# Performance work log

Hardware: AMD Instinct MI355X
Metric: run time of the kernel (lower is better)

Reference implementation:

```python
import jax, jax.numpy as jnp
import numpy as np

UPS_MEL = 100   # mel frame -> samples
UPS_LOW = 10    # lowres -> samples
H = 512         # GRU hidden
MEL = 80
LC = 20         # lowres conv channels
PRE = 256
SS = 30         # MOL sample_size (10 mixtures x 3)


def setup_inputs() -> dict:
    key = jax.random.key(0)
    ks = jax.random.split(key, 16)
    B, TM, TL = 8, 80, 800
    T = TM * UPS_MEL  # 8000
    rn = lambda k, s, sc=1.0: jax.random.normal(k, s, dtype=jnp.float32) * sc
    z = lambda n: jnp.zeros((n,), dtype=jnp.float32)
    return {
        "mel": rn(ks[0], (B, TM, MEL)),
        "x_low": rn(ks[1], (B, TL), 0.5),
        "gs_x": rn(ks[2], (B, T), 0.5),
        "conv_w0": rn(ks[3], (LC, 1, 7), 0.3),
        "conv_b0": z(LC),
        "conv_w1": rn(ks[4], (LC, LC, 7), 0.1),
        "conv_b1": z(LC),
        "conv_w2": rn(ks[5], (LC, LC, 7), 0.1),
        "conv_b2": z(LC),
        "gru_wih0": rn(ks[6], (3 * H, 102), 0.05),
        "gru_whh0": rn(ks[7], (3 * H, H), 0.05),
        "gru_bih0": z(3 * H),
        "gru_bhh0": z(3 * H),
        "gru_wih1": rn(ks[8], (3 * H, H), 0.05),
        "gru_whh1": rn(ks[9], (3 * H, H), 0.05),
        "gru_bih1": z(3 * H),
        "gru_bhh1": z(3 * H),
        "pre_w": rn(ks[10], (PRE, H), 0.05),
        "pre_b": z(PRE),
        "out_w": rn(ks[11], (SS, PRE), 0.05),
        "out_b": z(SS),
    }


def _lin_interp(x, out_len):
    # torch F.interpolate(mode='linear', align_corners=False) on [B, L] -> [B, out_len]
    L = x.shape[1]
    src = (jnp.arange(out_len, dtype=jnp.float32) + 0.5) * (L / out_len) - 0.5
    src = jnp.clip(src, 0.0, L - 1)
    i0 = jnp.floor(src).astype(jnp.int32)
    i1 = jnp.minimum(i0 + 1, L - 1)
    w = src - i0.astype(jnp.float32)
    return x[:, i0] * (1.0 - w) + x[:, i1] * w


def _conv1d(x, w, b):
    # x: [B, C, L], w: [O, I, K], 'same' padding (K=7 -> pad 3)
    k = w.shape[-1]
    p = (k - 1) // 2
    y = jax.lax.conv_general_dilated(x, w, (1,), [(p, p)],
                                     dimension_numbers=("NCH", "OIH", "NCH"))
    return y + b[None, :, None]


def _gru(x, wih, whh, bih, bhh):
    # x: [B, T, I] -> [B, T, H]; PyTorch GRU gate math, h0 = 0
    B = x.shape[0]
    xg = jnp.einsum("bti,gi->btg", x, wih) + bih  # [B, T, 3H]
    h0 = jnp.zeros((B, H), dtype=x.dtype)

    def step(h, xg_t):
        hg = h @ whh.T + bhh
        xr, xz, xn = jnp.split(xg_t, 3, axis=-1)
        hr, hz, hn = jnp.split(hg, 3, axis=-1)
        r = jax.nn.sigmoid(xr + hr)
        z = jax.nn.sigmoid(xz + hz)
        n = jnp.tanh(xn + r * hn)
        h_new = (1.0 - z) * n + z * h
        return h_new, h_new

    _, hs = jax.lax.scan(step, h0, jnp.swapaxes(xg, 0, 1))
    return jnp.swapaxes(hs, 0, 1)


def reference(mel, x_low, gs_x,
              conv_w0, conv_b0, conv_w1, conv_b1, conv_w2, conv_b2,
              gru_wih0, gru_whh0, gru_bih0, gru_bhh0,
              gru_wih1, gru_whh1, gru_bih1, gru_bhh1,
              pre_w, pre_b, out_w, out_b):
    # UpsampleNetR on mel: repeat each frame UPS_MEL times -> [B, T, 80]
    up_mel = jnp.repeat(mel, UPS_MEL, axis=1)
    # UpsampleNetI on x_low: linear interp x UPS_LOW -> [B, TL*10]
    interp_x = _lin_interp(x_low, x_low.shape[1] * UPS_LOW)
    # lowres conv stack with tanh: [B, 1, TL] -> [B, 20, TL]
    h = x_low[:, None, :]
    for w, b in ((conv_w0, conv_b0), (conv_w1, conv_b1), (conv_w2, conv_b2)):
        h = jnp.tanh(_conv1d(h, w, b))
    # UpsampleNetR on conv features: [B, TL, 20] repeated x10 -> [B, TL*10, 20]
    up_x = jnp.repeat(jnp.swapaxes(h, 1, 2), UPS_LOW, axis=1)

    msize = min(up_mel.shape[1], gs_x.shape[1], up_x.shape[1], interp_x.shape[1])
    hidden = jnp.concatenate([up_mel[:, :msize, :], up_x[:, :msize, :],
                              interp_x[:, :msize, None], gs_x[:, :msize, None]],
                             axis=-1)  # [B, T, 102]

    hidden = _gru(hidden, gru_wih0, gru_whh0, gru_bih0, gru_bhh0)
    hidden = _gru(hidden, gru_wih1, gru_whh1, gru_bih1, gru_bhh1)

    pre = jnp.tanh(hidden @ pre_w.T + pre_b)   # [B, T, 256]
    return pre @ out_w.T + out_b               # [B, T, 30]
```

## Files before the change

### kernel.cpp

```cpp
#include <hip/hip_runtime.h>
#include <hip/hip_fp16.h>
#include <stdint.h>

#define TT     8000
#define TLOW   800
#define TMEL   80
#define NMEL   80
#define NB     8
#define HD     512
#define LC     20
#define NPRE   256
#define NSS    30

#define HB_SLOTS (TT + 1)
#define HB_U64   ((size_t)HB_SLOTS * 8 * 128)
#define HB_BYTES (HB_U64 * 8)
#define CONV_BYTES   ((size_t)NB * TLOW * LC * 4)
#define INTERP_BYTES ((size_t)NB * TT * 4)
#define PREW16_BYTES ((size_t)NPRE * HD * 2)
#define OUTW16_BYTES ((size_t)NSS * NPRE * 2)

typedef __attribute__((ext_vector_type(8))) _Float16 half8;
typedef __attribute__((ext_vector_type(4))) float f32x4;

static __device__ __forceinline__ unsigned short f2h_bits(float f) {
    union { _Float16 h; unsigned short u; } c; c.h = (_Float16)f; return c.u;
}
static __device__ __forceinline__ float sigf(float x) {
    x = fminf(30.f, fmaxf(-30.f, x));
    return 1.f / (1.f + __expf(-x));
}
static __device__ __forceinline__ float tanhf_(float x) {
    x = fminf(15.f, fmaxf(-15.f, x));
    float e = __expf(2.f * x);
    return (e - 1.f) / (e + 1.f);
}
static __device__ __forceinline__ half8 mkfrag(unsigned long long a, unsigned long long b) {
    union { unsigned long long q[2]; half8 v; } u; u.q[0] = a; u.q[1] = b; return u.v;
}
static __device__ __forceinline__ f32x4 mfma(half8 a, half8 b, f32x4 c) {
    return __builtin_amdgcn_mfma_f32_16x16x32_f16(a, b, c, 0, 0, 0);
}

static __device__ __forceinline__ void issue16(const unsigned long long* __restrict__ p,
                                               int lane, unsigned long long* __restrict__ q)
{
    #pragma unroll
    for (int k = 0; k < 16; k++)
        q[k] = __hip_atomic_load(p + lane + 64 * k, __ATOMIC_RELAXED, __HIP_MEMORY_SCOPE_AGENT);
}
static __device__ __forceinline__ bool good16(const unsigned long long* __restrict__ q)
{
    bool bad = false;
    #pragma unroll
    for (int k = 0; k < 16; k++) {
        unsigned int lo = (unsigned int)q[k], hi = (unsigned int)(q[k] >> 32);
        bad |= (lo == 0xFFFFFFFFu) | (hi == 0xFFFFFFFFu);
    }
    return !__any(bad);
}
static __device__ __forceinline__ void stage16(unsigned long long* __restrict__ st,
                                               int lane, const unsigned long long* __restrict__ q)
{
    #pragma unroll
    for (int k = 0; k < 16; k++) { int i = lane + 64 * k; st[(i >> 7) * 129 + (i & 127)] = q[k]; }
}
static __device__ void poll_hot(const unsigned long long* __restrict__ slot,
                                int lane, unsigned long long* __restrict__ st)
{
    unsigned long long a[16], b[16];
    issue16(slot, lane, a);
    issue16(slot, lane, b);
    for (;;) {
        if (good16(a)) { stage16(st, lane, a); return; }
        issue16(slot, lane, a);
        if (good16(b)) { stage16(st, lane, b); return; }
        issue16(slot, lane, b);
    }
}
static __device__ void poll_sleep(const unsigned long long* __restrict__ slot,
                                  int lane, unsigned long long* __restrict__ st)
{
    unsigned long long a[16];
    for (;;) {
        issue16(slot, lane, a);
        if (good16(a)) break;
        __builtin_amdgcn_s_sleep(1);
    }
    stage16(st, lane, a);
}
static __device__ __forceinline__ half8 ldsfrag(const unsigned long long* __restrict__ st,
                                                int lane, int kt)
{
    int base = (lane & 7) * 129 + ((lane >> 4) << 1) + kt * 8;
    return mkfrag(st[base], st[base + 1]);
}

__global__ __launch_bounds__(256) void k_prep(
    const float* __restrict__ pre_w, const float* __restrict__ out_w,
    unsigned short* __restrict__ prew16, unsigned short* __restrict__ outw16)
{
    int i = blockIdx.x * 256 + threadIdx.x;
    if (i < NPRE * HD) prew16[i] = f2h_bits(pre_w[i]);
    if (i < NSS * NPRE) outw16[i] = f2h_bits(out_w[i]);
}

#define CHW 218
__global__ __launch_bounds__(256) void k_conv(
    const float* __restrict__ xlow,
    const float* __restrict__ w0, const float* __restrict__ cb0,
    const float* __restrict__ w1, const float* __restrict__ cb1,
    const float* __restrict__ w2, const float* __restrict__ cb2,
    float* __restrict__ convout, float* __restrict__ interp)
{
    int blk = blockIdx.x; int b = blk >> 2; int ch = blk & 3; int cb = ch * 200;
    int tid = threadIdx.x;
    __shared__ float xr[224];
    __shared__ float w0l[LC * 7], w1l[LC * LC * 7], w2l[LC * LC * 7];
    __shared__ float b0l[LC], b1l[LC], b2l[LC];
    __shared__ float h0[LC][CHW], h1[LC][CHW];

    for (int i = tid; i < LC * 7; i += 256) w0l[i] = w0[i];
    for (int i = tid; i < LC * LC * 7; i += 256) { w1l[i] = w1[i]; w2l[i] = w2[i]; }
    for (int i = tid; i < LC; i += 256) { b0l[i] = cb0[i]; b1l[i] = cb1[i]; b2l[i] = cb2[i]; }
    for (int i = tid; i < 224; i += 256) {
        int g = cb - 12 + i;
        xr[i] = (g >= 0 && g < TLOW) ? xlow[b * TLOW + g] : 0.f;
    }
    __syncthreads();
    for (int i = tid; i < LC * CHW; i += 256) {
        int c = i / CHW, s = i - c * CHW;
        int tg = cb - 9 + s;
        float a = b0l[c];
        #pragma unroll
        for (int j = 0; j < 7; j++) a += w0l[c * 7 + j] * xr[s + j];
        h0[c][s] = (tg >= 0 && tg < TLOW) ? tanhf_(a) : 0.f;
    }
    __syncthreads();
    for (int i = tid; i < LC * CHW; i += 256) {
        int c = i / CHW, s = i - c * CHW;
        int tg = cb - 9 + s;
        float a = b1l[c];
        for (int ci = 0; ci < LC; ci++) {
            #pragma unroll
            for (int j = 0; j < 7; j++) {
                int ss = s + j - 3;
                float hv = (ss >= 0 && ss < CHW) ? h0[ci][ss] : 0.f;
                a += w1l[(c * LC + ci) * 7 + j] * hv;
            }
        }
        h1[c][s] = (tg >= 0 && tg < TLOW) ? tanhf_(a) : 0.f;
    }
    __syncthreads();
    for (int i = tid; i < LC * 200; i += 256) {
        int c = i / 200, t0 = i - c * 200; int s = t0 + 9;
        float a = b2l[c];
        for (int ci = 0; ci < LC; ci++) {
            #pragma unroll
            for (int j = 0; j < 7; j++) a += w2l[(c * LC + ci) * 7 + j] * h1[ci][s + j - 3];
        }
        convout[((size_t)b * TLOW + cb + t0) * LC + c] = tanhf_(a);
    }
    for (int i = tid; i < 2000; i += 256) {
        int t = cb * 10 + i;
        float src = ((float)t + 0.5f) * 0.1f - 0.5f;
        src = fminf(fmaxf(src, 0.f), (float)(TLOW - 1));
        int i0 = (int)floorf(src); int i1 = (i0 + 1 < TLOW) ? i0 + 1 : TLOW - 1;
        float w = src - (float)i0;
        interp[(size_t)b * TT + t] = xlow[b * TLOW + i0] * (1.f - w) + xlow[b * TLOW + i1] * w;
    }
}

__global__ __launch_bounds__(384, 1) void k_rnn(
    const float* __restrict__ mel, const float* __restrict__ gsx,
    const float* __restrict__ convout, const float* __restrict__ interp,
    const float* __restrict__ wih0, const float* __restrict__ whh0,
    const float* __restrict__ bih0, const float* __restrict__ bhh0,
    const float* __restrict__ wih1, const float* __restrict__ whh1,
    const float* __restrict__ bih1, const float* __restrict__ bhh1,
    unsigned long long* __restrict__ h0buf, unsigned long long* __restrict__ h1buf)
{
    const int tid = threadIdx.x;
    const int wv = tid >> 6;
    const int lane = tid & 63;
    const int lm = lane & 15, lk = lane >> 4;
    const int g = wv >> 1;
    const int isH = wv & 1;
    const bool isL0 = (blockIdx.x < 32);
    const int cbid = isL0 ? blockIdx.x : (blockIdx.x - 32);
    const int cb = cbid * 16;
    const int row = g * 512 + cb + lm;

    __shared__ float exch[3][2][16][9];
    __shared__ __align__(16) unsigned short xv[2][16][136];
    __shared__ unsigned long long stX[8 * 129];
    __shared__ unsigned long long stH[8 * 129];

    const int cbb = lane >> 3;
    const int ci0 = (lane & 7) * 2, ci1 = ci0 + 1;
    float hr0 = 0.f, hr1 = 0.f;
    float bi0[3], bi1[3], bh0[3], bh1[3];
    if (wv == 0) {
        const float* bi = isL0 ? bih0 : bih1;
        const float* bh = isL0 ? bhh0 : bhh1;
        #pragma unroll
        for (int gg = 0; gg < 3; gg++) {
            bi0[gg] = bi[gg * 512 + cb + ci0]; bi1[gg] = bi[gg * 512 + cb + ci1];
            bh0[gg] = bh[gg * 512 + cb + ci0]; bh1[gg] = bh[gg * 512 + cb + ci1];
        }
    }
    for (int i = tid; i < 2 * 16 * 136; i += 384) (&xv[0][0][0])[i] = 0;

    if (wv == 0) {
        unsigned long long* buf = isL0 ? h0buf : h1buf;
        unsigned int* o32 = (unsigned int*)buf + (size_t)cbb * 256 + (cb >> 1) + (lane & 7);
        __hip_atomic_store(o32, 0u, __ATOMIC_RELAXED, __HIP_MEMORY_SCOPE_AGENT);
    }

    half8 wf[16];
    if (isL0) {
        if (!isH) {
            #pragma unroll
            for (int kt = 0; kt < 4; kt++)
                #pragma unroll
                for (int j = 0; j < 8; j++) {
                    int k = kt * 32 + lk * 8 + j;
                    wf[kt][j] = (k < 102) ? (_Float16)wih0[(size_t)row * 102 + k] : (_Float16)0.f;
                }
        } else {
            #pragma unroll
            for (int kt = 0; kt < 16; kt++)
                #pragma unroll
                for (int j = 0; j < 8; j++)
                    wf[kt][j] = (_Float16)whh0[(size_t)row * 512 + kt * 32 + lk * 8 + j];
        }
    } else {
        const float* wsrc = isH ? whh1 : wih1;
        #pragma unroll
        for (int kt = 0; kt < 16; kt++)
            #pragma unroll
            for (int j = 0; j < 8; j++)
                wf[kt][j] = (_Float16)wsrc[(size_t)row * 512 + kt * 32 + lk * 8 + j];
    }

    if (isL0) {
        {
            float pf[3];
            #pragma unroll
            for (int u = 0; u < 3; u++) {
                int e = tid + 384 * u; float v = 0.f;
                if (e < 816) {
                    int bb = e / 102, k = e - 102 * bb;
                    if (k < 80)       v = mel[((size_t)bb * TMEL + 0) * NMEL + k];
                    else if (k < 100) v = convout[((size_t)bb * TLOW + 0) * LC + (k - 80)];
                    else if (k == 100) v = interp[(size_t)bb * TT + 0];
                    else               v = gsx[(size_t)bb * TT + 0];
                }
                pf[u] = v;
            }
            #pragma unroll
            for (int u = 0; u < 3; u++) {
                int e = tid + 384 * u;
                if (e < 816) { int bb = e / 102, k = e - 102 * bb; xv[0][bb][k] = f2h_bits(pf[u]); }
            }
        }
        __syncthreads();

        for (int t = 0; t < TT; t++) {
            int tn = (t + 1 < TT) ? (t + 1) : (TT - 1);
            int tmi = tn / 100, tli = tn / 10;
            float pf[3];
            #pragma unroll
            for (int u = 0; u < 3; u++) {
                int e = tid + 384 * u; float v = 0.f;
                if (e < 816) {
                    int bb = e / 102, k = e - 102 * bb;
                    if (k < 80)       v = mel[((size_t)bb * TMEL + tmi) * NMEL + k];
                    else if (k < 100) v = convout[((size_t)bb * TLOW + tli) * LC + (k - 80)];
                    else if (k == 100) v = interp[(size_t)bb * TT + tn];
                    else               v = gsx[(size_t)bb * TT + tn];
                }
                pf[u] = v;
            }

            if (wv == 1) poll_hot(h0buf + (size_t)t * 1024, lane, stH);
            __syncthreads();

            if (!isH) {
                f32x4 acc = {0.f, 0.f, 0.f, 0.f};
                #pragma unroll
                for (int kt = 0; kt < 4; kt++) {
                    half8 xf = *(const half8*)&xv[t & 1][lm][kt * 32 + lk * 8];
                    acc = mfma(wf[kt], xf, acc);
                }
                if (lm < 8) {
                    #pragma unroll
                    for (int r2 = 0; r2 < 4; r2++) exch[g][0][lk * 4 + r2][lm] = acc[r2];
                }
            } else {
                f32x4 a0 = {0.f, 0.f, 0.f, 0.f}, a1 = {0.f, 0.f, 0.f, 0.f};
                #pragma unroll
                for (int i = 0; i < 8; i++) a0 = mfma(wf[i], ldsfrag(stH, lane, i), a0);
                #pragma unroll
                for (int i = 0; i < 8; i++) a1 = mfma(wf[8 + i], ldsfrag(stH, lane, 8 + i), a1);
                f32x4 acc = a0 + a1;
                if (lm < 8) {
                    #pragma unroll
                    for (int r2 = 0; r2 < 4; r2++) exch[g][1][lk * 4 + r2][lm] = acc[r2];
                }
            }
            #pragma unroll
            for (int u = 0; u < 3; u++) {
                int e = tid + 384 * u;
                if (e < 816) { int bb = e / 102, k = e - 102 * bb; xv[(t + 1) & 1][bb][k] = f2h_bits(pf[u]); }
            }
            __syncthreads();
            if (wv == 0) {
                float r0 = sigf(exch[0][0][ci0][cbb] + exch[0][1][ci0][cbb] + bi0[0] + bh0[0]);
                float z0 = sigf(exch[1][0][ci0][cbb] + exch[1][1][ci0][cbb] + bi0[1] + bh0[1]);
                float n0 = tanhf_(exch[2][0][ci0][cbb] + bi0[2] + r0 * (exch[2][1][ci0][cbb] + bh0[2]));
                hr0 = (1.f - z0) * n0 + z0 * hr0;
                float r1 = sigf(exch[0][0][ci1][cbb] + exch[0][1][ci1][cbb] + bi1[0] + bh1[0]);
                float z1 = sigf(exch[1][0][ci1][cbb] + exch[1][1][ci1][cbb] + bi1[1] + bh1[1]);
                float n1 = tanhf_(exch[2][0][ci1][cbb] + bi1[2] + r1 * (exch[2][1][ci1][cbb] + bh1[2]));
                hr1 = (1.f - z1) * n1 + z1 * hr1;
                unsigned int pk = (unsigned int)f2h_bits(hr0) | ((unsigned int)f2h_bits(hr1) << 16);
                unsigned int* o32 = (unsigned int*)(h0buf + (size_t)(t + 1) * 1024)
                                  + (size_t)cbb * 256 + (cb >> 1) + (lane & 7);
                __hip_atomic_store(o32, pk, __ATOMIC_RELAXED, __HIP_MEMORY_SCOPE_AGENT);
            }
        }
    } else {
        __syncthreads();
        for (int t = 0; t < TT; t++) {
            if (wv == 0)      poll_sleep(h0buf + (size_t)(t + 1) * 1024, lane, stX);
            else if (wv == 1) poll_hot(h1buf + (size_t)t * 1024, lane, stH);
            __syncthreads();

            const unsigned long long* src = isH ? stH : stX;
            f32x4 a0 = {0.f, 0.f, 0.f, 0.f}, a1 = {0.f, 0.f, 0.f, 0.f};
            #pragma unroll
            for (int i = 0; i < 8; i++) a0 = mfma(wf[i], ldsfrag(src, lane, i), a0);
            #pragma unroll
            for (int i = 0; i < 8; i++) a1 = mfma(wf[8 + i], ldsfrag(src, lane, 8 + i), a1);
            f32x4 acc = a0 + a1;
            if (lm < 8) {
                #pragma unroll
                for (int r2 = 0; r2 < 4; r2++) exch[g][isH][lk * 4 + r2][lm] = acc[r2];
            }
            __syncthreads();
            if (wv == 0) {
                float r0 = sigf(exch[0][0][ci0][cbb] + exch[0][1][ci0][cbb] + bi0[0] + bh0[0]);
                float z0 = sigf(exch[1][0][ci0][cbb] + exch[1][1][ci0][cbb] + bi0[1] + bh0[1]);
                float n0 = tanhf_(exch[2][0][ci0][cbb] + bi0[2] + r0 * (exch[2][1][ci0][cbb] + bh0[2]));
                hr0 = (1.f - z0) * n0 + z0 * hr0;
                float r1 = sigf(exch[0][0][ci1][cbb] + exch[0][1][ci1][cbb] + bi1[0] + bh1[0]);
                float z1 = sigf(exch[1][0][ci1][cbb] + exch[1][1][ci1][cbb] + bi1[1] + bh1[1]);
                float n1 = tanhf_(exch[2][0][ci1][cbb] + bi1[2] + r1 * (exch[2][1][ci1][cbb] + bh1[2]));
                hr1 = (1.f - z1) * n1 + z1 * hr1;
                unsigned int pk = (unsigned int)f2h_bits(hr0) | ((unsigned int)f2h_bits(hr1) << 16);
                unsigned int* o32 = (unsigned int*)(h1buf + (size_t)(t + 1) * 1024)
                                  + (size_t)cbb * 256 + (cb >> 1) + (lane & 7);
                __hip_atomic_store(o32, pk, __ATOMIC_RELAXED, __HIP_MEMORY_SCOPE_AGENT);
            }
        }
    }
}

__global__ __launch_bounds__(256) void k_final(
    const unsigned long long* __restrict__ h1buf,
    const unsigned short* __restrict__ prew16, const float* __restrict__ pre_b,
    const unsigned short* __restrict__ outw16, const float* __restrict__ out_b,
    float* __restrict__ out)
{
    int blk = blockIdx.x; int b = blk / 125; int tb = (blk - b * 125) * 64;
    int tid = threadIdx.x; int wv = tid >> 6; int l = tid & 63;
    int lm = l & 15, lk = l >> 4;

    half8 af[16];
    int trow = tb + wv * 16 + lm;
    const unsigned long long* abase = h1buf + ((size_t)(trow + 1) * 8 + b) * 128;
    #pragma unroll
    for (int kt = 0; kt < 16; kt++)
        af[kt] = mkfrag(abase[kt * 8 + lk * 2], abase[kt * 8 + lk * 2 + 1]);

    f32x4 acc[16];
    #pragma unroll
    for (int nt = 0; nt < 16; nt++) {
        f32x4 z = {0.f, 0.f, 0.f, 0.f}; acc[nt] = z;
        #pragma unroll
        for (int kt = 0; kt < 16; kt++) {
            int n = nt * 16 + lm; int k = kt * 32 + lk * 8;
            half8 bw = *(const half8*)&prew16[(size_t)n * HD + k];
            acc[nt] = mfma(af[kt], bw, acc[nt]);
        }
    }
    __shared__ __align__(16) unsigned short pt[64][264];
    #pragma unroll
    for (int nt = 0; nt < 16; nt++) {
        float pb = pre_b[nt * 16 + lm];
        #pragma unroll
        for (int r2 = 0; r2 < 4; r2++)
            pt[wv * 16 + lk * 4 + r2][nt * 16 + lm] = f2h_bits(tanhf_(acc[nt][r2] + pb));
    }
    __syncthreads();
    f32x4 a2[2];
    { f32x4 z = {0.f, 0.f, 0.f, 0.f}; a2[0] = z; a2[1] = z; }
    #pragma unroll
    for (int kt = 0; kt < 8; kt++) {
        half8 pa = *(const half8*)&pt[wv * 16 + lm][kt * 32 + lk * 8];
        #pragma unroll
        for (int nt = 0; nt < 2; nt++) {
            int n = nt * 16 + lm;
            half8 bw = (n < NSS) ? *(const half8*)&outw16[(size_t)n * NPRE + kt * 32 + lk * 8]
                                 : mkfrag(0ull, 0ull);
            a2[nt] = mfma(pa, bw, a2[nt]);
        }
    }
    #pragma unroll
    for (int nt = 0; nt < 2; nt++) {
        int n = nt * 16 + lm;
        if (n < NSS) {
            float ob = out_b[n];
            #pragma unroll
            for (int r2 = 0; r2 < 4; r2++) {
                int t = tb + wv * 16 + lk * 4 + r2;
                out[((size_t)b * TT + t) * NSS + n] = a2[nt][r2] + ob;
            }
        }
    }
}

extern "C" void kernel_launch(void* const* d_in, const int* in_sizes, int n_in,
                              void* d_out, int out_size, void* d_ws, size_t ws_size,
                              hipStream_t stream) {
    const float* mel  = (const float*)d_in[0];
    const float* xlow = (const float*)d_in[1];
    const float* gsx  = (const float*)d_in[2];
    const float* cw0  = (const float*)d_in[3];
    const float* cb0  = (const float*)d_in[4];
    const float* cw1  = (const float*)d_in[5];
    const float* cb1  = (const float*)d_in[6];
    const float* cw2  = (const float*)d_in[7];
    const float* cb2  = (const float*)d_in[8];
    const float* wih0 = (const float*)d_in[9];
    const float* whh0 = (const float*)d_in[10];
    const float* bih0 = (const float*)d_in[11];
    const float* bhh0 = (const float*)d_in[12];
    const float* wih1 = (const float*)d_in[13];
    const float* whh1 = (const float*)d_in[14];
    const float* bih1 = (const float*)d_in[15];
    const float* bhh1 = (const float*)d_in[16];
    const float* prew = (const float*)d_in[17];
    const float* preb = (const float*)d_in[18];
    const float* outw = (const float*)d_in[19];
    const float* outb = (const float*)d_in[20];

    size_t needed = 2 * HB_BYTES + CONV_BYTES + INTERP_BYTES + PREW16_BYTES + OUTW16_BYTES;
    if (ws_size < needed) return;

    char* ws = (char*)d_ws;
    unsigned long long* h0buf = (unsigned long long*)ws;
    unsigned long long* h1buf = (unsigned long long*)(ws + HB_BYTES);
    float* convout = (float*)(ws + 2 * HB_BYTES);
    float* interp  = (float*)(ws + 2 * HB_BYTES + CONV_BYTES);
    unsigned short* prew16 = (unsigned short*)(ws + 2 * HB_BYTES + CONV_BYTES + INTERP_BYTES);
    unsigned short* outw16 = (unsigned short*)(ws + 2 * HB_BYTES + CONV_BYTES + INTERP_BYTES + PREW16_BYTES);

    hipMemsetAsync(ws, 0xFF, 2 * HB_BYTES, stream);

    k_prep<<<(NPRE * HD + 255) / 256, 256, 0, stream>>>(prew, outw, prew16, outw16);
    k_conv<<<32, 256, 0, stream>>>(xlow, cw0, cb0, cw1, cb1, cw2, cb2, convout, interp);
    k_rnn<<<64, 384, 0, stream>>>(mel, gsx, convout, interp,
                                  wih0, whh0, bih0, bhh0,
                                  wih1, whh1, bih1, bhh1,
                                  h0buf, h1buf);
    k_final<<<1000, 256, 0, stream>>>(h1buf, prew16, preb, outw16, outb, (float*)d_out);
}
```

Before: 21.18 ms.

## Halve RNN block count with 32-column blocks and rebalanced MFMA work split

The persistent GRU kernel moves from 64 blocks of 384 threads, each owning 16 hidden columns, to 32 blocks of 768 threads, each owning 32 columns. In layer 0 the input projection and the recurrent K dimension are split more evenly across waves, with a third partial-sum slot in the exchange buffer. The hot double-buffered poller is replaced by a single sleeping poller. Fewer blocks means fewer producers and consumers on the cross-block handshake each step, but per-block barriers now cover more waves and the sleep-based polling may add latency.

```diff
diff --git a/kernel.cpp b/kernel.cpp
--- a/kernel.cpp
+++ b/kernel.cpp
@@ -59,35 +59,17 @@
     }
     return !__any(bad);
 }
-static __device__ __forceinline__ void stage16(unsigned long long* __restrict__ st,
-                                               int lane, const unsigned long long* __restrict__ q)
-{
+static __device__ void poll_stage(const unsigned long long* __restrict__ slot,
+                                  int lane, unsigned long long* __restrict__ st)
+{
+    unsigned long long q[16];
+    for (;;) {
+        issue16(slot, lane, q);
+        if (good16(q)) break;
+        __builtin_amdgcn_s_sleep(1);
+    }
     #pragma unroll
     for (int k = 0; k < 16; k++) { int i = lane + 64 * k; st[(i >> 7) * 129 + (i & 127)] = q[k]; }
-}
-static __device__ void poll_hot(const unsigned long long* __restrict__ slot,
-                                int lane, unsigned long long* __restrict__ st)
-{
-    unsigned long long a[16], b[16];
-    issue16(slot, lane, a);
-    issue16(slot, lane, b);
-    for (;;) {
-        if (good16(a)) { stage16(st, lane, a); return; }
-        issue16(slot, lane, a);
-        if (good16(b)) { stage16(st, lane, b); return; }
-        issue16(slot, lane, b);
-    }
-}
-static __device__ void poll_sleep(const unsigned long long* __restrict__ slot,
-                                  int lane, unsigned long long* __restrict__ st)
-{
-    unsigned long long a[16];
-    for (;;) {
-        issue16(slot, lane, a);
-        if (good16(a)) break;
-        __builtin_amdgcn_s_sleep(1);
-    }
-    stage16(st, lane, a);
 }
 static __device__ __forceinline__ half8 ldsfrag(const unsigned long long* __restrict__ st,
                                                 int lane, int kt)
@@ -171,7 +153,7 @@
     }
 }
 
-__global__ __launch_bounds__(384, 1) void k_rnn(
+__global__ __launch_bounds__(768, 1) void k_rnn(
     const float* __restrict__ mel, const float* __restrict__ gsx,
     const float* __restrict__ convout, const float* __restrict__ interp,
     const float* __restrict__ wih0, const float* __restrict__ whh0,
@@ -184,71 +166,59 @@
     const int wv = tid >> 6;
     const int lane = tid & 63;
     const int lm = lane & 15, lk = lane >> 4;
-    const int g = wv >> 1;
-    const int isH = wv & 1;
-    const bool isL0 = (blockIdx.x < 32);
-    const int cbid = isL0 ? blockIdx.x : (blockIdx.x - 32);
-    const int cb = cbid * 16;
-    const int row = g * 512 + cb + lm;
-
-    __shared__ float exch[3][2][16][9];
+    const int g = wv >> 2;
+    const int sub = wv & 3;
+    const bool isL0 = (blockIdx.x < 16);
+    const int cbid = isL0 ? blockIdx.x : (blockIdx.x - 16);
+    const int cb = cbid * 32;
+
+    __shared__ float exch[3][3][32][9];
     __shared__ __align__(16) unsigned short xv[2][16][136];
     __shared__ unsigned long long stX[8 * 129];
     __shared__ unsigned long long stH[8 * 129];
 
     const int cbb = lane >> 3;
-    const int ci0 = (lane & 7) * 2, ci1 = ci0 + 1;
+    const int ci0 = wv * 16 + (lane & 7) * 2;
     float hr0 = 0.f, hr1 = 0.f;
     float bi0[3], bi1[3], bh0[3], bh1[3];
-    if (wv == 0) {
+    if (wv < 2) {
         const float* bi = isL0 ? bih0 : bih1;
         const float* bh = isL0 ? bhh0 : bhh1;
         #pragma unroll
         for (int gg = 0; gg < 3; gg++) {
-            bi0[gg] = bi[gg * 512 + cb + ci0]; bi1[gg] = bi[gg * 512 + cb + ci1];
-            bh0[gg] = bh[gg * 512 + cb + ci0]; bh1[gg] = bh[gg * 512 + cb + ci1];
-        }
-    }
-    for (int i = tid; i < 2 * 16 * 136; i += 384) (&xv[0][0][0])[i] = 0;
-
-    if (wv == 0) {
+            bi0[gg] = bi[gg * 512 + cb + ci0];     bi1[gg] = bi[gg * 512 + cb + ci0 + 1];
+            bh0[gg] = bh[gg * 512 + cb + ci0];     bh1[gg] = bh[gg * 512 + cb + ci0 + 1];
+        }
+    }
+    for (int i = tid; i < 2 * 16 * 136; i += 768) (&xv[0][0][0])[i] = 0;
+
+    if (wv < 2) {
         unsigned long long* buf = isL0 ? h0buf : h1buf;
-        unsigned int* o32 = (unsigned int*)buf + (size_t)cbb * 256 + (cb >> 1) + (lane & 7);
+        unsigned int* o32 = (unsigned int*)buf + (size_t)cbb * 256 + cbid * 16 + wv * 8 + (lane & 7);
         __hip_atomic_store(o32, 0u, __ATOMIC_RELAXED, __HIP_MEMORY_SCOPE_AGENT);
     }
 
-    half8 wf[16];
     if (isL0) {
-        if (!isH) {
-            #pragma unroll
-            for (int kt = 0; kt < 4; kt++)
-                #pragma unroll
-                for (int j = 0; j < 8; j++) {
-                    int k = kt * 32 + lk * 8 + j;
-                    wf[kt][j] = (k < 102) ? (_Float16)wih0[(size_t)row * 102 + k] : (_Float16)0.f;
-                }
-        } else {
-            #pragma unroll
-            for (int kt = 0; kt < 16; kt++)
-                #pragma unroll
-                for (int j = 0; j < 8; j++)
-                    wf[kt][j] = (_Float16)whh0[(size_t)row * 512 + kt * 32 + lk * 8 + j];
-        }
-    } else {
-        const float* wsrc = isH ? whh1 : wih1;
-        #pragma unroll
-        for (int kt = 0; kt < 16; kt++)
-            #pragma unroll
-            for (int j = 0; j < 8; j++)
-                wf[kt][j] = (_Float16)wsrc[(size_t)row * 512 + kt * 32 + lk * 8 + j];
-    }
-
-    if (isL0) {
+        const int mt = sub >> 1, kh = sub & 1;
+        const int row = g * 512 + cb + mt * 16 + lm;
+        half8 wf[10];
+        #pragma unroll
+        for (int q = 0; q < 10; q++) {
+            #pragma unroll
+            for (int j = 0; j < 8; j++) {
+                float v;
+                if (kh == 0) {
+                    if (q < 4) { int k = q * 32 + lk * 8 + j; v = (k < 102) ? wih0[(size_t)row * 102 + k] : 0.f; }
+                    else       { int k = (q - 4) * 32 + lk * 8 + j; v = whh0[(size_t)row * 512 + k]; }
+                } else       { int k = (q + 6) * 32 + lk * 8 + j; v = whh0[(size_t)row * 512 + k]; }
+                wf[q][j] = (_Float16)v;
+            }
+        }
         {
-            float pf[3];
-            #pragma unroll
-            for (int u = 0; u < 3; u++) {
-                int e = tid + 384 * u; float v = 0.f;
+            float pf[2];
+            #pragma unroll
+            for (int u = 0; u < 2; u++) {
+                int e = tid + 768 * u; float v = 0.f;
                 if (e < 816) {
                     int bb = e / 102, k = e - 102 * bb;
                     if (k < 80)       v = mel[((size_t)bb * TMEL + 0) * NMEL + k];
@@ -259,8 +229,8 @@
                 pf[u] = v;
             }
             #pragma unroll
-            for (int u = 0; u < 3; u++) {
-                int e = tid + 384 * u;
+            for (int u = 0; u < 2; u++) {
+                int e = tid + 768 * u;
                 if (e < 816) { int bb = e / 102, k = e - 102 * bb; xv[0][bb][k] = f2h_bits(pf[u]); }
             }
         }
@@ -269,10 +239,10 @@
         for (int t = 0; t < TT; t++) {
             int tn = (t + 1 < TT) ? (t + 1) : (TT - 1);
             int tmi = tn / 100, tli = tn / 10;
-            float pf[3];
-            #pragma unroll
-            for (int u = 0; u < 3; u++) {
-                int e = tid + 384 * u; float v = 0.f;
+            float pf[2];
+            #pragma unroll
+            for (int u = 0; u < 2; u++) {
+                int e = tid + 768 * u; float v = 0.f;
                 if (e < 816) {
                     int bb = e / 102, k = e - 102 * bb;
                     if (k < 80)       v = mel[((size_t)bb * TMEL + tmi) * NMEL + k];
@@ -283,84 +253,103 @@
                 pf[u] = v;
             }
 
-            if (wv == 1) poll_hot(h0buf + (size_t)t * 1024, lane, stH);
+            if (wv == 3) poll_stage(h0buf + (size_t)t * 1024, lane, stH);
             __syncthreads();
 
-            if (!isH) {
-                f32x4 acc = {0.f, 0.f, 0.f, 0.f};
+            if (kh == 0) {
+                f32x4 aX = {0.f, 0.f, 0.f, 0.f}, aH = {0.f, 0.f, 0.f, 0.f};
                 #pragma unroll
-                for (int kt = 0; kt < 4; kt++) {
-                    half8 xf = *(const half8*)&xv[t & 1][lm][kt * 32 + lk * 8];
-                    acc = mfma(wf[kt], xf, acc);
+                for (int q = 0; q < 4; q++) {
+                    half8 xf = *(const half8*)&xv[t & 1][lm][q * 32 + lk * 8];
+                    aX = mfma(wf[q], xf, aX);
                 }
+                #pragma unroll
+                for (int q = 0; q < 6; q++) aH = mfma(wf[4 + q], ldsfrag(stH, lane, q), aH);
                 if (lm < 8) {
                     #pragma unroll
-                    for (int r2 = 0; r2 < 4; r2++) exch[g][0][lk * 4 + r2][lm] = acc[r2];
+                    for (int r2 = 0; r2 < 4; r2++) {
+                        exch[g][0][mt * 16 + lk * 4 + r2][lm] = aX[r2];
+                        exch[g][1][mt * 16 + lk * 4 + r2][lm] = aH[r2];
+                    }
                 }
             } else {
-                f32x4 a0 = {0.f, 0.f, 0.f, 0.f}, a1 = {0.f, 0.f, 0.f, 0.f};
+                f32x4 aH = {0.f, 0.f, 0.f, 0.f}, aH2 = {0.f, 0.f, 0.f, 0.f};
                 #pragma unroll
-                for (int i = 0; i < 8; i++) a0 = mfma(wf[i], ldsfrag(stH, lane, i), a0);
+                for (int q = 0; q < 5; q++) aH = mfma(wf[q], ldsfrag(stH, lane, 6 + q), aH);
                 #pragma unroll
-                for (int i = 0; i < 8; i++) a1 = mfma(wf[8 + i], ldsfrag(stH, lane, 8 + i), a1);
-                f32x4 acc = a0 + a1;
+                for (int q = 5; q < 10; q++) aH2 = mfma(wf[q], ldsfrag(stH, lane, 6 + q), aH2);
+                aH = aH + aH2;
                 if (lm < 8) {
                     #pragma unroll
-                    for (int r2 = 0; r2 < 4; r2++) exch[g][1][lk * 4 + r2][lm] = acc[r2];
+                    for (int r2 = 0; r2 < 4; r2++) exch[g][2][mt * 16 + lk * 4 + r2][lm] = aH[r2];
                 }
             }
             #pragma unroll
-            for (int u = 0; u < 3; u++) {
-                int e = tid + 384 * u;
+            for (int u = 0; u < 2; u++) {
+                int e = tid + 768 * u;
                 if (e < 816) { int bb = e / 102, k = e - 102 * bb; xv[(t + 1) & 1][bb][k] = f2h_bits(pf[u]); }
             }
             __syncthreads();
-            if (wv == 0) {
+            if (wv < 2) {
+                float r0 = sigf(exch[0][0][ci0][cbb] + exch[0][1][ci0][cbb] + exch[0][2][ci0][cbb] + bi0[0] + bh0[0]);
+                float z0 = sigf(exch[1][0][ci0][cbb] + exch[1][1][ci0][cbb] + exch[1][2][ci0][cbb] + bi0[1] + bh0[1]);
+                float n0 = tanhf_(exch[2][0][ci0][cbb] + bi0[2]
+                                  + r0 * (exch[2][1][ci0][cbb] + exch[2][2][ci0][cbb] + bh0[2]));
+                hr0 = (1.f - z0) * n0 + z0 * hr0;
+                int i1 = ci0 + 1;
+                float r1 = sigf(exch[0][0][i1][cbb] + exch[0][1][i1][cbb] + exch[0][2][i1][cbb] + bi1[0] + bh1[0]);
+                float z1 = sigf(exch[1][0][i1][cbb] + exch[1][1][i1][cbb] + exch[1][2][i1][cbb] + bi1[1] + bh1[1]);
+                float n1 = tanhf_(exch[2][0][i1][cbb] + bi1[2]
+                                  + r1 * (exch[2][1][i1][cbb] + exch[2][2][i1][cbb] + bh1[2]));
+                hr1 = (1.f - z1) * n1 + z1 * hr1;
+                unsigned int pk = (unsigned int)f2h_bits(hr0) | ((unsigned int)f2h_bits(hr1) << 16);
+                unsigned int* o32 = (unsigned int*)(h0buf + (size_t)(t + 1) * 1024)
+                                  + (size_t)cbb * 256 + cbid * 16 + wv * 8 + (lane & 7);
+                __hip_atomic_store(o32, pk, __ATOMIC_RELAXED, __HIP_MEMORY_SCOPE_AGENT);
+            }
+        }
+    } else {
+        const int isH = sub >> 1, mt = sub & 1;
+        const int row = g * 512 + cb + mt * 16 + lm;
+        const float* wsrc = isH ? whh1 : wih1;
+        half8 wf[16];
+        #pragma unroll
+        for (int q = 0; q < 16; q++)
+            #pragma unroll
+            for (int j = 0; j < 8; j++)
+                wf[q][j] = (_Float16)wsrc[(size_t)row * 512 + q * 32 + lk * 8 + j];
+        __syncthreads();
+
+        for (int t = 0; t < TT; t++) {
+            if (wv == 2)      poll_stage(h0buf + (size_t)(t + 1) * 1024, lane, stX);
+            else if (wv == 3) poll_stage(h1buf + (size_t)t * 1024,       lane, stH);
+            __syncthreads();
+
+            const unsigned long long* src = isH ? stH : stX;
+            f32x4 a0 = {0.f, 0.f, 0.f, 0.f}, a1 = {0.f, 0.f, 0.f, 0.f};
+            #pragma unroll
+            for (int q = 0; q < 8; q++) a0 = mfma(wf[q], ldsfrag(src, lane, q), a0);
+            #pragma unroll
+            for (int q = 8; q < 16; q++) a1 = mfma(wf[q], ldsfrag(src, lane, q), a1);
+            f32x4 acc = a0 + a1;
+            if (lm < 8) {
+                #pragma unroll
+                for (int r2 = 0; r2 < 4; r2++) exch[g][isH][mt * 16 + lk * 4 + r2][lm] = acc[r2];
+            }
+            __syncthreads();
+            if (wv < 2) {
                 float r0 = sigf(exch[0][0][ci0][cbb] + exch[0][1][ci0][cbb] + bi0[0] + bh0[0]);
                 float z0 = sigf(exch[1][0][ci0][cbb] + exch[1][1][ci0][cbb] + bi0[1] + bh0[1]);
                 float n0 = tanhf_(exch[2][0][ci0][cbb] + bi0[2] + r0 * (exch[2][1][ci0][cbb] + bh0[2]));
                 hr0 = (1.f - z0) * n0 + z0 * hr0;
-                float r1 = sigf(exch[0][0][ci1][cbb] + exch[0][1][ci1][cbb] + bi1[0] + bh1[0]);
-                float z1 = sigf(exch[1][0][ci1][cbb] + exch[1][1][ci1][cbb] + bi1[1] + bh1[1]);
-                float n1 = tanhf_(exch[2][0][ci1][cbb] + bi1[2] + r1 * (exch[2][1][ci1][cbb] + bh1[2]));
-                hr1 = (1.f - z1) * n1 + z1 * hr1;
-                unsigned int pk = (unsigned int)f2h_bits(hr0) | ((unsigned int)f2h_bits(hr1) << 16);
-                unsigned int* o32 = (unsigned int*)(h0buf + (size_t)(t + 1) * 1024)
-                                  + (size_t)cbb * 256 + (cb >> 1) + (lane & 7);
-                __hip_atomic_store(o32, pk, __ATOMIC_RELAXED, __HIP_MEMORY_SCOPE_AGENT);
-            }
-        }
-    } else {
-        __syncthreads();
-        for (int t = 0; t < TT; t++) {
-            if (wv == 0)      poll_sleep(h0buf + (size_t)(t + 1) * 1024, lane, stX);
-            else if (wv == 1) poll_hot(h1buf + (size_t)t * 1024, lane, stH);
-            __syncthreads();
-
-            const unsigned long long* src = isH ? stH : stX;
-            f32x4 a0 = {0.f, 0.f, 0.f, 0.f}, a1 = {0.f, 0.f, 0.f, 0.f};
-            #pragma unroll
-            for (int i = 0; i < 8; i++) a0 = mfma(wf[i], ldsfrag(src, lane, i), a0);
-            #pragma unroll
-            for (int i = 0; i < 8; i++) a1 = mfma(wf[8 + i], ldsfrag(src, lane, 8 + i), a1);
-            f32x4 acc = a0 + a1;
-            if (lm < 8) {
-                #pragma unroll
-                for (int r2 = 0; r2 < 4; r2++) exch[g][isH][lk * 4 + r2][lm] = acc[r2];
-            }
-            __syncthreads();
-            if (wv == 0) {
-                float r0 = sigf(exch[0][0][ci0][cbb] + exch[0][1][ci0][cbb] + bi0[0] + bh0[0]);
-                float z0 = sigf(exch[1][0][ci0][cbb] + exch[1][1][ci0][cbb] + bi0[1] + bh0[1]);
-                float n0 = tanhf_(exch[2][0][ci0][cbb] + bi0[2] + r0 * (exch[2][1][ci0][cbb] + bh0[2]));
-                hr0 = (1.f - z0) * n0 + z0 * hr0;
-                float r1 = sigf(exch[0][0][ci1][cbb] + exch[0][1][ci1][cbb] + bi1[0] + bh1[0]);
-                float z1 = sigf(exch[1][0][ci1][cbb] + exch[1][1][ci1][cbb] + bi1[1] + bh1[1]);
-                float n1 = tanhf_(exch[2][0][ci1][cbb] + bi1[2] + r1 * (exch[2][1][ci1][cbb] + bh1[2]));
+                int i1 = ci0 + 1;
+                float r1 = sigf(exch[0][0][i1][cbb] + exch[0][1][i1][cbb] + bi1[0] + bh1[0]);
+                float z1 = sigf(exch[1][0][i1][cbb] + exch[1][1][i1][cbb] + bi1[1] + bh1[1]);
+                float n1 = tanhf_(exch[2][0][i1][cbb] + bi1[2] + r1 * (exch[2][1][i1][cbb] + bh1[2]));
                 hr1 = (1.f - z1) * n1 + z1 * hr1;
                 unsigned int pk = (unsigned int)f2h_bits(hr0) | ((unsigned int)f2h_bits(hr1) << 16);
                 unsigned int* o32 = (unsigned int*)(h1buf + (size_t)(t + 1) * 1024)
-                                  + (size_t)cbb * 256 + (cb >> 1) + (lane & 7);
+                                  + (size_t)cbb * 256 + cbid * 16 + wv * 8 + (lane & 7);
                 __hip_atomic_store(o32, pk, __ATOMIC_RELAXED, __HIP_MEMORY_SCOPE_AGENT);
             }
         }
@@ -471,7 +460,7 @@
 
     k_prep<<<(NPRE * HD + 255) / 256, 256, 0, stream>>>(prew, outw, prew16, outw16);
     k_conv<<<32, 256, 0, stream>>>(xlow, cw0, cb0, cw1, cb1, cw2, cb2, convout, interp);
-    k_rnn<<<64, 384, 0, stream>>>(mel, gsx, convout, interp,
+    k_rnn<<<32, 768, 0, stream>>>(mel, gsx, convout, interp,
                                   wih0, whh0, bih0, bhh0,
                                   wih1, whh1, bih1, bhh1,
                                   h0buf, h1buf);
```

Measured after the change: 20.98 ms. No clear change (-1.0%).
